# Performance work log

Hardware: AMD Instinct MI355X
Metric: run time of the kernel (lower is better)

Reference implementation:

```python
import jax, jax.numpy as jnp
import numpy as np

KERNEL = 8
STRIDE = 4
HEADS = 8
DIM = 512


def setup_inputs() -> dict:
    key = jax.random.key(0)
    ks = jax.random.split(key, 6)
    B, H, W, C = 8, 64, 64, DIM
    hd = C // HEADS
    return {
        "x": jax.random.normal(ks[0], (B, H, W, C), jnp.float32),
        "w_qkv": jax.random.normal(ks[1], (3 * C, C), jnp.float32) * (C ** -0.5),
        "w_out": jax.random.normal(ks[2], (C, C), jnp.float32) * (C ** -0.5),
        "b_out": jax.random.normal(ks[3], (C,), jnp.float32) * 0.01,
        "rel_h": jax.random.normal(ks[4], (KERNEL, hd), jnp.float32),
        "rel_w": jax.random.normal(ks[5], (KERNEL, hd), jnp.float32),
    }


def reference(x, w_qkv, w_out, b_out, rel_h, rel_w):
    B, H, W, C = x.shape
    k, s, heads = KERNEL, STRIDE, HEADS
    hd = C // heads
    scale = hd ** -0.5
    nH = (H - k) // s + 1
    nW = (W - k) // s + 1
    L = k * k

    # window gather indices
    ii = (jnp.arange(nH) * s)[:, None] + jnp.arange(k)  # [nH, k]
    jj = (jnp.arange(nW) * s)[:, None] + jnp.arange(k)  # [nW, k]
    Ai = ii[:, None, :, None]  # [nH,1,k,1]
    Aj = jj[None, :, None, :]  # [1,nW,1,k]

    win = x[:, Ai, Aj, :]  # [B, nH, nW, k, k, C]
    # faithful to source: permute(0,3,1,2).reshape(B,-1,C) scrambles C into tokens
    xv = jnp.moveaxis(win, -1, 3).reshape(B, nH, nW, L, C)  # [B,nH,nW,L,C]

    qkv = jnp.einsum('bnwlc,oc->bnwlo', xv, w_qkv)  # [B,nH,nW,L,3C]
    q, kk, v = jnp.split(qkv, 3, axis=-1)
    def heads_split(t):
        return t.reshape(B, nH, nW, L, heads, hd)
    q, kk, v = heads_split(q), heads_split(kk), heads_split(v)

    dots = jnp.einsum('bnwlhd,bnwmhd->bnwhlm', q, kk) * scale  # [B,nH,nW,h,L,L]
    # relative bias: (q @ rel^T).sum over kernel axis, broadcast over key dim
    bias_h = jnp.einsum('bnwlhd,kd->bnwhlk', q, rel_h).sum(-1)  # [B,nH,nW,h,L]
    bias_w = jnp.einsum('bnwlhd,kd->bnwhlk', q, rel_w).sum(-1)
    dots = dots + (bias_h + bias_w)[..., None]

    attn = jax.nn.softmax(dots, axis=-1)
    out = jnp.einsum('bnwhlm,bnwmhd->bnwlhd', attn, v).reshape(B, nH, nW, L, C)
    out = jnp.einsum('bnwlc,oc->bnwlo', out, w_out) + b_out  # to_out

    # faithful undo of buggy layout: reshape(B,C,k,k).permute(0,2,3,1)
    out = jnp.moveaxis(out.reshape(B, nH, nW, C, k, k), 3, -1)  # [B,nH,nW,k,k,C]

    res = jnp.zeros_like(x).at[:, Ai, Aj, :].add(out)  # overlapping += accumulation
    return res
```

## Files before the change

kernel.cpp:

```cpp
#include <hip/hip_runtime.h>

#define NHW 15

typedef __bf16 bf16x8 __attribute__((ext_vector_type(8)));
typedef float f32x4 __attribute__((ext_vector_type(4)));
typedef unsigned short u16x8 __attribute__((ext_vector_type(8)));

__device__ __forceinline__ unsigned short f2bf(float f) {
  unsigned x = __float_as_uint(f);
  unsigned r = ((x >> 16) & 1u) + 0x7fffu;
  x += r;
  return (unsigned short)(x >> 16);
}

__device__ __forceinline__ unsigned cvtpk(float lo, float hi) {
  unsigned r;
  asm("v_cvt_pk_bf16_f32 %0, %1, %2" : "=v"(r) : "v"(lo), "v"(hi));
  return r;
}

__global__ void convert_weights(const float* __restrict__ wq,
                                const float* __restrict__ wo,
                                unsigned short* __restrict__ dst) {
  int t = blockIdx.x * 256 + threadIdx.x;
  if (t < 98304) {
    int lane = t & 63, nt = (t >> 6) & 3, ks = (t >> 8) & 15, g = t >> 12;
    int o = g * 64 + nt * 16 + (lane & 15);
    int a = ks * 4 + (lane >> 4);
    const float* src = wq + (size_t)o * 512 + a;
    u16x8 v;
    #pragma unroll
    for (int e = 0; e < 8; ++e) v[e] = f2bf(src[e * 64]);
    *(u16x8*)(dst + (size_t)t * 8) = v;
  } else {
    int u = t - 98304;
    int lane = u & 63, nt = (u >> 6) & 3, ks = (u >> 8) & 15, g = u >> 12;
    int o = g * 64 + nt * 16 + (lane & 15);
    int c0 = ks * 32 + (lane >> 4) * 8;
    const float* src = wo + (size_t)o * 512 + c0;
    float4 v0 = *(const float4*)(src);
    float4 v1 = *(const float4*)(src + 4);
    u16x8 pk;
    pk[0] = f2bf(v0.x); pk[1] = f2bf(v0.y); pk[2] = f2bf(v0.z); pk[3] = f2bf(v0.w);
    pk[4] = f2bf(v1.x); pk[5] = f2bf(v1.y); pk[6] = f2bf(v1.z); pk[7] = f2bf(v1.w);
    *(u16x8*)(dst + 786432 + (size_t)u * 8) = pk;
  }
}

__launch_bounds__(512)
__global__ void swin_kernel(const float* __restrict__ x,
                            const float* __restrict__ b_out,
                            const unsigned short* __restrict__ wq_all,
                            const unsigned short* __restrict__ wo,
                            float* __restrict__ res,
                            int n0, int w0, int nN, int nW, int do_add) {
  __shared__ __align__(16) unsigned short lds0[40960];

  const int tid  = threadIdx.x;
  const int wave = tid >> 6;
  const int ln   = tid & 63;
  const int rowa = ln & 15;
  const int kgrp = ln >> 4;
  const int rbase = kgrp * 4;

  const int bid = blockIdx.x;
  const int b  = bid / (nN * nW);
  const int rm = bid % (nN * nW);
  const int n  = n0 + 2 * (rm / nW);
  const int w  = w0 + 2 * (rm % nW);
  const int i0 = n * 4, j0 = w * 4;

  {
    const float* src = x + (((size_t)(b * 64 + i0)) * 64 + j0 + wave) * 512 + 8 * ln;
    float4 v0[8], v1[8];
    #pragma unroll
    for (int r = 0; r < 8; ++r) {
      v0[r] = *(const float4*)(src + (size_t)r * 32768);
      v1[r] = *(const float4*)(src + (size_t)r * 32768 + 4);
    }
    #pragma unroll
    for (int r = 0; r < 8; ++r) {
      uint4 pk;
      pk.x = cvtpk(v0[r].x, v0[r].y);
      pk.y = cvtpk(v0[r].z, v0[r].w);
      pk.z = cvtpk(v1[r].x, v1[r].y);
      pk.w = cvtpk(v1[r].z, v1[r].w);
      *(uint4*)(lds0 + ln * 520 + (r * 8 + wave) * 8) = pk;
    }
  }
  __syncthreads();

  unsigned qp[4][4][2], kp[4][4][2], vp[4][4][2];
  {
    auto step = [&](int g, unsigned (&dst)[4][4][2]) {
      f32x4 acc[4][4];
      #pragma unroll
      for (int i = 0; i < 4; ++i)
        #pragma unroll
        for (int j = 0; j < 4; ++j) acc[i][j] = (f32x4){0.f, 0.f, 0.f, 0.f};
      const unsigned short* wb = wq_all + (size_t)g * 32768 + ln * 8;
      bf16x8 b0[4], b1[4];
      #pragma unroll
      for (int nt = 0; nt < 4; ++nt) b0[nt] = *(const bf16x8*)(wb + (0 * 4 + nt) * 512);
      #pragma unroll
      for (int nt = 0; nt < 4; ++nt) b1[nt] = *(const bf16x8*)(wb + (1 * 4 + nt) * 512);
      #pragma unroll 1
      for (int ks2 = 0; ks2 < 8; ++ks2) {
        bf16x8 bn0[4], bn1[4];
        if (ks2 < 7) {
          #pragma unroll
          for (int nt = 0; nt < 4; ++nt)
            bn0[nt] = *(const bf16x8*)(wb + ((2 * ks2 + 2) * 4 + nt) * 512);
          #pragma unroll
          for (int nt = 0; nt < 4; ++nt)
            bn1[nt] = *(const bf16x8*)(wb + ((2 * ks2 + 3) * 4 + nt) * 512);
        }
        bf16x8 a[4];
        #pragma unroll
        for (int mt = 0; mt < 4; ++mt)
          a[mt] = *(const bf16x8*)(lds0 + (mt * 16 + rowa) * 520 + (2 * ks2) * 32 + kgrp * 8);
        __builtin_amdgcn_s_setprio(1);
        #pragma unroll
        for (int nt = 0; nt < 4; ++nt)
          #pragma unroll
          for (int mt = 0; mt < 4; ++mt)
            acc[mt][nt] = __builtin_amdgcn_mfma_f32_16x16x32_bf16(a[mt], b0[nt], acc[mt][nt], 0, 0, 0);
        __builtin_amdgcn_s_setprio(0);
        #pragma unroll
        for (int mt = 0; mt < 4; ++mt)
          a[mt] = *(const bf16x8*)(lds0 + (mt * 16 + rowa) * 520 + (2 * ks2 + 1) * 32 + kgrp * 8);
        __builtin_amdgcn_s_setprio(1);
        #pragma unroll
        for (int nt = 0; nt < 4; ++nt)
          #pragma unroll
          for (int mt = 0; mt < 4; ++mt)
            acc[mt][nt] = __builtin_amdgcn_mfma_f32_16x16x32_bf16(a[mt], b1[nt], acc[mt][nt], 0, 0, 0);
        __builtin_amdgcn_s_setprio(0);
        if (ks2 < 7) {
          #pragma unroll
          for (int nt = 0; nt < 4; ++nt) { b0[nt] = bn0[nt]; b1[nt] = bn1[nt]; }
        }
      }
      #pragma unroll
      for (int mt = 0; mt < 4; ++mt)
        #pragma unroll
        for (int nt = 0; nt < 4; ++nt)
          #pragma unroll
          for (int p = 0; p < 2; ++p)
            dst[mt][nt][p] = cvtpk(acc[mt][nt][2 * p], acc[mt][nt][2 * p + 1]);
    };
    step(wave,      qp);
    step(8 + wave,  kp);
    step(16 + wave, vp);
  }
  __syncthreads();

  unsigned short* qsc = lds0 + wave * 5120;
  unsigned short* ksc = qsc + 2560;

  f32x4 dt_[4][4];
  #pragma unroll
  for (int i = 0; i < 4; ++i)
    #pragma unroll
    for (int j = 0; j < 4; ++j) dt_[i][j] = (f32x4){0.f, 0.f, 0.f, 0.f};

  #pragma unroll
  for (int h2 = 0; h2 < 2; ++h2) {
    #pragma unroll
    for (int mt = 0; mt < 4; ++mt)
      #pragma unroll
      for (int cc = 0; cc < 2; ++cc) {
        int ct = 2 * h2 + cc;
        #pragma unroll
        for (int p = 0; p < 2; ++p) {
          unsigned uq = qp[mt][ct][p];
          unsigned uk = kp[mt][ct][p];
          int rr = mt * 16 + rbase + 2 * p;
          int dd = cc * 16 + rowa;
          qsc[rr * 40 + dd]       = (unsigned short)uq;
          qsc[(rr + 1) * 40 + dd] = (unsigned short)(uq >> 16);
          ksc[rr * 40 + dd]       = (unsigned short)uk;
          ksc[(rr + 1) * 40 + dd] = (unsigned short)(uk >> 16);
        }
      }
    bf16x8 aq[4];
    #pragma unroll
    for (int mt = 0; mt < 4; ++mt)
      aq[mt] = *(const bf16x8*)(qsc + (mt * 16 + rowa) * 40 + kgrp * 8);
    __builtin_amdgcn_s_setprio(1);
    #pragma unroll
    for (int nt = 0; nt < 4; ++nt) {
      bf16x8 bk = *(const bf16x8*)(ksc + (nt * 16 + rowa) * 40 + kgrp * 8);
      #pragma unroll
      for (int mt = 0; mt < 4; ++mt)
        dt_[mt][nt] = __builtin_amdgcn_mfma_f32_16x16x32_bf16(aq[mt], bk, dt_[mt][nt], 0, 0, 0);
    }
    __builtin_amdgcn_s_setprio(0);
  }

  const float SC = 0.125f * 1.44269504088896f;
  float rsum[4][4];
  #pragma unroll
  for (int mt = 0; mt < 4; ++mt)
    #pragma unroll
    for (int j = 0; j < 4; ++j) {
      float m = dt_[mt][0][j];
      #pragma unroll
      for (int nt = 1; nt < 4; ++nt) m = fmaxf(m, dt_[mt][nt][j]);
      #pragma unroll
      for (int s = 1; s < 16; s <<= 1) m = fmaxf(m, __shfl_xor(m, s, 64));
      float sum = 0.f;
      #pragma unroll
      for (int nt = 0; nt < 4; ++nt) {
        float p = exp2f((dt_[mt][nt][j] - m) * SC);
        dt_[mt][nt][j] = p;
        sum += p;
      }
      #pragma unroll
      for (int s = 1; s < 16; s <<= 1) sum += __shfl_xor(sum, s, 64);
      rsum[mt][j] = sum;
    }

  unsigned short* Psc  = qsc;
  unsigned short* vTsc = ksc;
  f32x4 oat[4][4];
  #pragma unroll
  for (int i = 0; i < 4; ++i)
    #pragma unroll
    for (int j = 0; j < 4; ++j) oat[i][j] = (f32x4){0.f, 0.f, 0.f, 0.f};

  #pragma unroll
  for (int mh = 0; mh < 2; ++mh) {
    #pragma unroll
    for (int mt = 0; mt < 4; ++mt)
      #pragma unroll
      for (int cc = 0; cc < 2; ++cc) {
        int ct = 2 * mh + cc;
        #pragma unroll
        for (int j = 0; j < 4; ++j)
          Psc[(mt * 16 + rbase + j) * 40 + cc * 16 + rowa] = f2bf(dt_[mt][ct][j]);
      }
    #pragma unroll
    for (int mm = 0; mm < 2; ++mm) {
      int mtm = 2 * mh + mm;
      #pragma unroll
      for (int ct = 0; ct < 4; ++ct)
        #pragma unroll
        for (int p = 0; p < 2; ++p) {
          unsigned u = vp[mtm][ct][p];
          int m_ = mm * 16 + rbase + 2 * p;
          int d  = ct * 16 + rowa;
          *(unsigned*)(vTsc + d * 40 + m_) = u;
        }
    }
    bf16x8 ap[4];
    #pragma unroll
    for (int mt = 0; mt < 4; ++mt)
      ap[mt] = *(const bf16x8*)(Psc + (mt * 16 + rowa) * 40 + kgrp * 8);
    __builtin_amdgcn_s_setprio(1);
    #pragma unroll
    for (int dtt = 0; dtt < 4; ++dtt) {
      bf16x8 bv = *(const bf16x8*)(vTsc + (dtt * 16 + rowa) * 40 + kgrp * 8);
      #pragma unroll
      for (int mt = 0; mt < 4; ++mt)
        oat[mt][dtt] = __builtin_amdgcn_mfma_f32_16x16x32_bf16(ap[mt], bv, oat[mt][dtt], 0, 0, 0);
    }
    __builtin_amdgcn_s_setprio(0);
  }

  #pragma unroll
  for (int mt = 0; mt < 4; ++mt)
    #pragma unroll
    for (int j = 0; j < 4; ++j) {
      float inv = 1.f / rsum[mt][j];
      int l = mt * 16 + rbase + j;
      #pragma unroll
      for (int dtt = 0; dtt < 4; ++dtt)
        qsc[l * 72 + dtt * 16 + rowa] = f2bf(oat[mt][dtt][j] * inv);
    }
  __syncthreads();

  f32x4 a2[4][4];
  #pragma unroll
  for (int i = 0; i < 4; ++i)
    #pragma unroll
    for (int j = 0; j < 4; ++j) a2[i][j] = (f32x4){0.f, 0.f, 0.f, 0.f};
  {
    const unsigned short* wb = wo + (size_t)wave * 32768 + ln * 8;
    bf16x8 b0[4], b1[4];
    #pragma unroll
    for (int nt = 0; nt < 4; ++nt) b0[nt] = *(const bf16x8*)(wb + (0 * 4 + nt) * 512);
    #pragma unroll
    for (int nt = 0; nt < 4; ++nt) b1[nt] = *(const bf16x8*)(wb + (1 * 4 + nt) * 512);
    #pragma unroll 1
    for (int ks2 = 0; ks2 < 8; ++ks2) {
      bf16x8 bn0[4], bn1[4];
      if (ks2 < 7) {
        #pragma unroll
        for (int nt = 0; nt < 4; ++nt)
          bn0[nt] = *(const bf16x8*)(wb + ((2 * ks2 + 2) * 4 + nt) * 512);
        #pragma unroll
        for (int nt = 0; nt < 4; ++nt)
          bn1[nt] = *(const bf16x8*)(wb + ((2 * ks2 + 3) * 4 + nt) * 512);
      }
      bf16x8 a[4];
      #pragma unroll
      for (int mt = 0; mt < 4; ++mt)
        a[mt] = *(const bf16x8*)(lds0 + ks2 * 5120 + (mt * 16 + rowa) * 72 + kgrp * 8);
      __builtin_amdgcn_s_setprio(1);
      #pragma unroll
      for (int nt = 0; nt < 4; ++nt)
        #pragma unroll
        for (int mt = 0; mt < 4; ++mt)
          a2[mt][nt] = __builtin_amdgcn_mfma_f32_16x16x32_bf16(a[mt], b0[nt], a2[mt][nt], 0, 0, 0);
      __builtin_amdgcn_s_setprio(0);
      #pragma unroll
      for (int mt = 0; mt < 4; ++mt)
        a[mt] = *(const bf16x8*)(lds0 + ks2 * 5120 + (mt * 16 + rowa) * 72 + 32 + kgrp * 8);
      __builtin_amdgcn_s_setprio(1);
      #pragma unroll
      for (int nt = 0; nt < 4; ++nt)
        #pragma unroll
        for (int mt = 0; mt < 4; ++mt)
          a2[mt][nt] = __builtin_amdgcn_mfma_f32_16x16x32_bf16(a[mt], b1[nt], a2[mt][nt], 0, 0, 0);
      __builtin_amdgcn_s_setprio(0);
      if (ks2 < 7) {
        #pragma unroll
        for (int nt = 0; nt < 4; ++nt) { b0[nt] = bn0[nt]; b1[nt] = bn1[nt]; }
      }
    }
  }

  float bias[4];
  #pragma unroll
  for (int nt = 0; nt < 4; ++nt) bias[nt] = b_out[wave * 64 + nt * 16 + rowa];

  __syncthreads();

  float* fl = (float*)lds0;
  #pragma unroll
  for (int ph = 0; ph < 2; ++ph) {
    float4 vold[8];
    if (do_add) {
      #pragma unroll
      for (int it = 0; it < 8; ++it) {
        int idx = it * 512 + tid;
        int pp  = idx >> 7;
        int c4  = (idx & 127) << 2;
        int p   = ph * 32 + pp;
        int gh = i0 + (p >> 3), gw = j0 + (p & 7);
        vold[it] = *(const float4*)(res + (((size_t)(b * 64 + gh)) * 64 + gw) * 512 + c4);
      }
    }
    if (ph) __syncthreads();
    #pragma unroll
    for (int nt2 = 0; nt2 < 2; ++nt2) {
      int nt = 2 * ph + nt2;
      int prow = nt2 * 16 + rowa;
      #pragma unroll
      for (int mt = 0; mt < 4; ++mt)
        #pragma unroll
        for (int j = 0; j < 4; ++j) {
          int ch = (mt * 16 + rbase + j) * 8 + wave;
          fl[prow * 517 + ch] = a2[mt][nt][j] + bias[nt];
        }
    }
    __syncthreads();
    #pragma unroll
    for (int it = 0; it < 8; ++it) {
      int idx = it * 512 + tid;
      int pp  = idx >> 7;
      int c4  = (idx & 127) << 2;
      float4 v = *(const float4*)(fl + pp * 517 + c4);
      int p  = ph * 32 + pp;
      int gh = i0 + (p >> 3), gw = j0 + (p & 7);
      float* dst = res + (((size_t)(b * 64 + gh)) * 64 + gw) * 512 + c4;
      if (do_add) {
        v.x += vold[it].x; v.y += vold[it].y; v.z += vold[it].z; v.w += vold[it].w;
      }
      *(float4*)dst = v;
    }
  }
}

extern "C" void kernel_launch(void* const* d_in, const int* in_sizes, int n_in,
                              void* d_out, int out_size, void* d_ws, size_t ws_size,
                              hipStream_t stream) {
  const float* x      = (const float*)d_in[0];
  const float* w_qkv  = (const float*)d_in[1];
  const float* w_out  = (const float*)d_in[2];
  const float* b_out  = (const float*)d_in[3];
  float* res = (float*)d_out;
  unsigned short* wbf = (unsigned short*)d_ws;

  convert_weights<<<512, 256, 0, stream>>>(w_qkv, w_out, wbf);

  const int cls[4][5] = {
      {0, 0, 8, 8, 0},
      {0, 1, 8, 7, 1},
      {1, 0, 7, 8, 1},
      {1, 1, 7, 7, 1},
  };
  for (int c = 0; c < 4; ++c) {
    int nblk = 8 * cls[c][2] * cls[c][3];
    swin_kernel<<<nblk, 512, 0, stream>>>(x, b_out, wbf, wbf + 786432, res,
                                          cls[c][0], cls[c][1], cls[c][2],
                                          cls[c][3], cls[c][4]);
  }
}
```

Before: 380.9 us.

## Split fused window kernel into separate QKV GEMM and attention kernels

Replaces the single fused per-window kernel with two kernels. The first is a QKV projection GEMM that tiles four windows per block across twelve N-blocks and writes bf16 QKV fragments to a workspace buffer. The second is an attention-plus-output-projection kernel that reads those fragments back. The aim is better parallelism and weight reuse in the projection, which dominates the work, at the cost of extra global traffic for the intermediate and more launches. It falls back to the old fused kernel when the workspace is too small.

```diff
diff --git a/kernel.cpp b/kernel.cpp
--- a/kernel.cpp
+++ b/kernel.cpp
@@ -47,6 +47,367 @@
   }
 }
 
+__launch_bounds__(512, 4)
+__global__ void gemm_qkv(const float* __restrict__ x,
+                         const unsigned short* __restrict__ wq_all,
+                         unsigned* __restrict__ qkv,
+                         int n0, int w0, int nN, int nW, int off) {
+  __shared__ __align__(16) unsigned short xs[256 * 72];
+
+  const int tid  = threadIdx.x;
+  const int wave = tid >> 6;
+  const int ln   = tid & 63;
+  const int rowa = ln & 15;
+  const int kgrp = ln >> 4;
+  const int mg = blockIdx.x / 12;
+  const int nb = blockIdx.x % 12;
+  const int awin = wave >> 1;
+  const int wn   = wave & 1;
+  const int g    = nb * 2 + wn;
+
+  int bb[4], i0a[4], j0a[4];
+  {
+    const int nNW = nN * nW;
+    #pragma unroll
+    for (int q = 0; q < 4; ++q) {
+      int rm = off + mg * 4 + q;
+      int b  = rm / nNW;
+      int r1 = rm % nNW;
+      bb[q]  = b;
+      i0a[q] = (n0 + 2 * (r1 / nW)) * 4;
+      j0a[q] = (w0 + 2 * (r1 % nW)) * 4;
+    }
+  }
+
+  f32x4 acc[4][4];
+  #pragma unroll
+  for (int i = 0; i < 4; ++i)
+    #pragma unroll
+    for (int j = 0; j < 4; ++j) acc[i][j] = (f32x4){0.f, 0.f, 0.f, 0.f};
+
+  const unsigned short* wb = wq_all + (size_t)g * 32768 + ln * 8;
+
+  for (int r = 0; r < 8; ++r) {
+    __syncthreads();
+    #pragma unroll
+    for (int q = 0; q < 4; ++q) {
+      const float* src =
+          x + (((size_t)(bb[q] * 64 + i0a[q] + r)) * 64 + j0a[q] + wave) * 512 + 8 * ln;
+      float4 v0 = *(const float4*)(src);
+      float4 v1 = *(const float4*)(src + 4);
+      uint4 pk;
+      pk.x = cvtpk(v0.x, v0.y);
+      pk.y = cvtpk(v0.z, v0.w);
+      pk.z = cvtpk(v1.x, v1.y);
+      pk.w = cvtpk(v1.z, v1.w);
+      *(uint4*)(xs + (q * 64 + ln) * 72 + wave * 8) = pk;
+    }
+    __syncthreads();
+    #pragma unroll
+    for (int kk = 0; kk < 2; ++kk) {
+      const int ks = 2 * r + kk;
+      bf16x8 bfr[4];
+      #pragma unroll
+      for (int nt = 0; nt < 4; ++nt)
+        bfr[nt] = *(const bf16x8*)(wb + (size_t)(ks * 4 + nt) * 512);
+      bf16x8 a[4];
+      #pragma unroll
+      for (int mt = 0; mt < 4; ++mt)
+        a[mt] = *(const bf16x8*)(xs + (awin * 64 + mt * 16 + rowa) * 72 + kk * 32 + kgrp * 8);
+      __builtin_amdgcn_s_setprio(1);
+      #pragma unroll
+      for (int nt = 0; nt < 4; ++nt)
+        #pragma unroll
+        for (int mt = 0; mt < 4; ++mt)
+          acc[mt][nt] = __builtin_amdgcn_mfma_f32_16x16x32_bf16(a[mt], bfr[nt], acc[mt][nt], 0, 0, 0);
+      __builtin_amdgcn_s_setprio(0);
+    }
+  }
+
+  unsigned img[32];
+  #pragma unroll
+  for (int mt = 0; mt < 4; ++mt)
+    #pragma unroll
+    for (int nt = 0; nt < 4; ++nt)
+      #pragma unroll
+      for (int p = 0; p < 2; ++p)
+        img[(mt * 4 + nt) * 2 + p] = cvtpk(acc[mt][nt][2 * p], acc[mt][nt][2 * p + 1]);
+  unsigned* dst = qkv + (((size_t)(mg * 4 + awin) * 24 + g) * 64 + ln) * 32;
+  #pragma unroll
+  for (int k = 0; k < 8; ++k) {
+    uint4 v;
+    v.x = img[4 * k]; v.y = img[4 * k + 1]; v.z = img[4 * k + 2]; v.w = img[4 * k + 3];
+    *(uint4*)(dst + 4 * k) = v;
+  }
+}
+
+__launch_bounds__(512)
+__global__ void attn_kernel(const float* __restrict__ b_out,
+                            const unsigned short* __restrict__ wo,
+                            const unsigned* __restrict__ qkv,
+                            float* __restrict__ res,
+                            int n0, int w0, int nN, int nW, int off, int do_add) {
+  __shared__ __align__(16) unsigned short lds0[40960];
+
+  const int tid  = threadIdx.x;
+  const int wave = tid >> 6;
+  const int ln   = tid & 63;
+  const int rowa = ln & 15;
+  const int kgrp = ln >> 4;
+  const int rbase = kgrp * 4;
+
+  const int rml = blockIdx.x;
+  const int rmg = off + rml;
+  const int b  = rmg / (nN * nW);
+  const int r1 = rmg % (nN * nW);
+  const int n  = n0 + 2 * (r1 / nW);
+  const int w  = w0 + 2 * (r1 % nW);
+  const int i0 = n * 4, j0 = w * 4;
+
+  unsigned qp[4][4][2], kp[4][4][2], vp[4][4][2];
+  {
+    const unsigned* base = qkv + ((size_t)rml * 24 * 64 + ln) * 32;
+    #pragma unroll
+    for (int mt = 0; mt < 4; ++mt)
+      #pragma unroll
+      for (int nt = 0; nt < 4; ++nt)
+        #pragma unroll
+        for (int p = 0; p < 2; ++p) {
+          int idx = (mt * 4 + nt) * 2 + p;
+          qp[mt][nt][p] = base[((size_t)(wave)      * 64) * 32 + idx];
+          kp[mt][nt][p] = base[((size_t)(8 + wave)  * 64) * 32 + idx];
+          vp[mt][nt][p] = base[((size_t)(16 + wave) * 64) * 32 + idx];
+        }
+  }
+
+  unsigned short* qsc = lds0 + wave * 5120;
+  unsigned short* ksc = qsc + 2560;
+
+  f32x4 dt_[4][4];
+  #pragma unroll
+  for (int i = 0; i < 4; ++i)
+    #pragma unroll
+    for (int j = 0; j < 4; ++j) dt_[i][j] = (f32x4){0.f, 0.f, 0.f, 0.f};
+
+  #pragma unroll
+  for (int h2 = 0; h2 < 2; ++h2) {
+    #pragma unroll
+    for (int mt = 0; mt < 4; ++mt)
+      #pragma unroll
+      for (int cc = 0; cc < 2; ++cc) {
+        int ct = 2 * h2 + cc;
+        #pragma unroll
+        for (int p = 0; p < 2; ++p) {
+          unsigned uq = qp[mt][ct][p];
+          unsigned uk = kp[mt][ct][p];
+          int rr = mt * 16 + rbase + 2 * p;
+          int dd = cc * 16 + rowa;
+          qsc[rr * 40 + dd]       = (unsigned short)uq;
+          qsc[(rr + 1) * 40 + dd] = (unsigned short)(uq >> 16);
+          ksc[rr * 40 + dd]       = (unsigned short)uk;
+          ksc[(rr + 1) * 40 + dd] = (unsigned short)(uk >> 16);
+        }
+      }
+    bf16x8 aq[4];
+    #pragma unroll
+    for (int mt = 0; mt < 4; ++mt)
+      aq[mt] = *(const bf16x8*)(qsc + (mt * 16 + rowa) * 40 + kgrp * 8);
+    __builtin_amdgcn_s_setprio(1);
+    #pragma unroll
+    for (int nt = 0; nt < 4; ++nt) {
+      bf16x8 bk = *(const bf16x8*)(ksc + (nt * 16 + rowa) * 40 + kgrp * 8);
+      #pragma unroll
+      for (int mt = 0; mt < 4; ++mt)
+        dt_[mt][nt] = __builtin_amdgcn_mfma_f32_16x16x32_bf16(aq[mt], bk, dt_[mt][nt], 0, 0, 0);
+    }
+    __builtin_amdgcn_s_setprio(0);
+  }
+
+  const float SC = 0.125f * 1.44269504088896f;
+  float rsum[4][4];
+  #pragma unroll
+  for (int mt = 0; mt < 4; ++mt)
+    #pragma unroll
+    for (int j = 0; j < 4; ++j) {
+      float m = dt_[mt][0][j];
+      #pragma unroll
+      for (int nt = 1; nt < 4; ++nt) m = fmaxf(m, dt_[mt][nt][j]);
+      #pragma unroll
+      for (int s = 1; s < 16; s <<= 1) m = fmaxf(m, __shfl_xor(m, s, 64));
+      float sum = 0.f;
+      #pragma unroll
+      for (int nt = 0; nt < 4; ++nt) {
+        float p = exp2f((dt_[mt][nt][j] - m) * SC);
+        dt_[mt][nt][j] = p;
+        sum += p;
+      }
+      #pragma unroll
+      for (int s = 1; s < 16; s <<= 1) sum += __shfl_xor(sum, s, 64);
+      rsum[mt][j] = sum;
+    }
+
+  unsigned short* Psc  = qsc;
+  unsigned short* vTsc = ksc;
+  f32x4 oat[4][4];
+  #pragma unroll
+  for (int i = 0; i < 4; ++i)
+    #pragma unroll
+    for (int j = 0; j < 4; ++j) oat[i][j] = (f32x4){0.f, 0.f, 0.f, 0.f};
+
+  #pragma unroll
+  for (int mh = 0; mh < 2; ++mh) {
+    #pragma unroll
+    for (int mt = 0; mt < 4; ++mt)
+      #pragma unroll
+      for (int cc = 0; cc < 2; ++cc) {
+        int ct = 2 * mh + cc;
+        #pragma unroll
+        for (int j = 0; j < 4; ++j)
+          Psc[(mt * 16 + rbase + j) * 40 + cc * 16 + rowa] = f2bf(dt_[mt][ct][j]);
+      }
+    #pragma unroll
+    for (int mm = 0; mm < 2; ++mm) {
+      int mtm = 2 * mh + mm;
+      #pragma unroll
+      for (int ct = 0; ct < 4; ++ct)
+        #pragma unroll
+        for (int p = 0; p < 2; ++p) {
+          unsigned u = vp[mtm][ct][p];
+          int m_ = mm * 16 + rbase + 2 * p;
+          int d  = ct * 16 + rowa;
+          *(unsigned*)(vTsc + d * 40 + m_) = u;
+        }
+    }
+    bf16x8 ap[4];
+    #pragma unroll
+    for (int mt = 0; mt < 4; ++mt)
+      ap[mt] = *(const bf16x8*)(Psc + (mt * 16 + rowa) * 40 + kgrp * 8);
+    __builtin_amdgcn_s_setprio(1);
+    #pragma unroll
+    for (int dtt = 0; dtt < 4; ++dtt) {
+      bf16x8 bv = *(const bf16x8*)(vTsc + (dtt * 16 + rowa) * 40 + kgrp * 8);
+      #pragma unroll
+      for (int mt = 0; mt < 4; ++mt)
+        oat[mt][dtt] = __builtin_amdgcn_mfma_f32_16x16x32_bf16(ap[mt], bv, oat[mt][dtt], 0, 0, 0);
+    }
+    __builtin_amdgcn_s_setprio(0);
+  }
+
+  #pragma unroll
+  for (int mt = 0; mt < 4; ++mt)
+    #pragma unroll
+    for (int j = 0; j < 4; ++j) {
+      float inv = 1.f / rsum[mt][j];
+      int l = mt * 16 + rbase + j;
+      #pragma unroll
+      for (int dtt = 0; dtt < 4; ++dtt)
+        qsc[l * 72 + dtt * 16 + rowa] = f2bf(oat[mt][dtt][j] * inv);
+    }
+  __syncthreads();
+
+  f32x4 a2[4][4];
+  #pragma unroll
+  for (int i = 0; i < 4; ++i)
+    #pragma unroll
+    for (int j = 0; j < 4; ++j) a2[i][j] = (f32x4){0.f, 0.f, 0.f, 0.f};
+  {
+    const unsigned short* wb = wo + (size_t)wave * 32768 + ln * 8;
+    bf16x8 b0[4], b1[4];
+    #pragma unroll
+    for (int nt = 0; nt < 4; ++nt) b0[nt] = *(const bf16x8*)(wb + (0 * 4 + nt) * 512);
+    #pragma unroll
+    for (int nt = 0; nt < 4; ++nt) b1[nt] = *(const bf16x8*)(wb + (1 * 4 + nt) * 512);
+    #pragma unroll 1
+    for (int ks2 = 0; ks2 < 8; ++ks2) {
+      bf16x8 bn0[4], bn1[4];
+      if (ks2 < 7) {
+        #pragma unroll
+        for (int nt = 0; nt < 4; ++nt)
+          bn0[nt] = *(const bf16x8*)(wb + ((2 * ks2 + 2) * 4 + nt) * 512);
+        #pragma unroll
+        for (int nt = 0; nt < 4; ++nt)
+          bn1[nt] = *(const bf16x8*)(wb + ((2 * ks2 + 3) * 4 + nt) * 512);
+      }
+      bf16x8 a[4];
+      #pragma unroll
+      for (int mt = 0; mt < 4; ++mt)
+        a[mt] = *(const bf16x8*)(lds0 + ks2 * 5120 + (mt * 16 + rowa) * 72 + kgrp * 8);
+      __builtin_amdgcn_s_setprio(1);
+      #pragma unroll
+      for (int nt = 0; nt < 4; ++nt)
+        #pragma unroll
+        for (int mt = 0; mt < 4; ++mt)
+          a2[mt][nt] = __builtin_amdgcn_mfma_f32_16x16x32_bf16(a[mt], b0[nt], a2[mt][nt], 0, 0, 0);
+      __builtin_amdgcn_s_setprio(0);
+      #pragma unroll
+      for (int mt = 0; mt < 4; ++mt)
+        a[mt] = *(const bf16x8*)(lds0 + ks2 * 5120 + (mt * 16 + rowa) * 72 + 32 + kgrp * 8);
+      __builtin_amdgcn_s_setprio(1);
+      #pragma unroll
+      for (int nt = 0; nt < 4; ++nt)
+        #pragma unroll
+        for (int mt = 0; mt < 4; ++mt)
+          a2[mt][nt] = __builtin_amdgcn_mfma_f32_16x16x32_bf16(a[mt], b1[nt], a2[mt][nt], 0, 0, 0);
+      __builtin_amdgcn_s_setprio(0);
+      if (ks2 < 7) {
+        #pragma unroll
+        for (int nt = 0; nt < 4; ++nt) { b0[nt] = bn0[nt]; b1[nt] = bn1[nt]; }
+      }
+    }
+  }
+
+  float bias[4];
+  #pragma unroll
+  for (int nt = 0; nt < 4; ++nt) bias[nt] = b_out[wave * 64 + nt * 16 + rowa];
+
+  __syncthreads();
+
+  float* fl = (float*)lds0;
+  #pragma unroll
+  for (int ph = 0; ph < 2; ++ph) {
+    float4 vold[8];
+    if (do_add) {
+      #pragma unroll
+      for (int it = 0; it < 8; ++it) {
+        int idx = it * 512 + tid;
+        int pp  = idx >> 7;
+        int c4  = (idx & 127) << 2;
+        int p   = ph * 32 + pp;
+        int gh = i0 + (p >> 3), gw = j0 + (p & 7);
+        vold[it] = *(const float4*)(res + (((size_t)(b * 64 + gh)) * 64 + gw) * 512 + c4);
+      }
+    }
+    if (ph) __syncthreads();
+    #pragma unroll
+    for (int nt2 = 0; nt2 < 2; ++nt2) {
+      int nt = 2 * ph + nt2;
+      int prow = nt2 * 16 + rowa;
+      #pragma unroll
+      for (int mt = 0; mt < 4; ++mt)
+        #pragma unroll
+        for (int j = 0; j < 4; ++j) {
+          int ch = (mt * 16 + rbase + j) * 8 + wave;
+          fl[prow * 517 + ch] = a2[mt][nt][j] + bias[nt];
+        }
+    }
+    __syncthreads();
+    #pragma unroll
+    for (int it = 0; it < 8; ++it) {
+      int idx = it * 512 + tid;
+      int pp  = idx >> 7;
+      int c4  = (idx & 127) << 2;
+      float4 v = *(const float4*)(fl + pp * 517 + c4);
+      int p  = ph * 32 + pp;
+      int gh = i0 + (p >> 3), gw = j0 + (p & 7);
+      float* dst = res + (((size_t)(b * 64 + gh)) * 64 + gw) * 512 + c4;
+      if (do_add) {
+        v.x += vold[it].x; v.y += vold[it].y; v.z += vold[it].z; v.w += vold[it].w;
+      }
+      *(float4*)dst = v;
+    }
+  }
+}
+
 __launch_bounds__(512)
 __global__ void swin_kernel(const float* __restrict__ x,
                             const float* __restrict__ b_out,
@@ -392,6 +753,7 @@
   const float* b_out  = (const float*)d_in[3];
   float* res = (float*)d_out;
   unsigned short* wbf = (unsigned short*)d_ws;
+  unsigned* qkvbuf = (unsigned*)((char*)d_ws + (2u << 20));
 
   convert_weights<<<512, 256, 0, stream>>>(w_qkv, w_out, wbf);
 
@@ -401,10 +763,33 @@
       {1, 0, 7, 8, 1},
       {1, 1, 7, 7, 1},
   };
-  for (int c = 0; c < 4; ++c) {
-    int nblk = 8 * cls[c][2] * cls[c][3];
-    swin_kernel<<<nblk, 512, 0, stream>>>(x, b_out, wbf, wbf + 786432, res,
-                                          cls[c][0], cls[c][1], cls[c][2],
-                                          cls[c][3], cls[c][4]);
+
+  const size_t base = (size_t)2 << 20;
+  const size_t per_win = (size_t)24 * 64 * 32 * 4;
+  int chunks;
+  if (ws_size >= base + 512 * per_win)      chunks = 1;
+  else if (ws_size >= base + 256 * per_win) chunks = 2;
+  else                                      chunks = 0;
+
+  if (chunks > 0) {
+    for (int c = 0; c < 4; ++c) {
+      int nwin = 8 * cls[c][2] * cls[c][3];
+      int per = nwin / chunks;
+      for (int h = 0; h < chunks; ++h) {
+        int off = h * per;
+        gemm_qkv<<<(per / 4) * 12, 512, 0, stream>>>(
+            x, wbf, qkvbuf, cls[c][0], cls[c][1], cls[c][2], cls[c][3], off);
+        attn_kernel<<<per, 512, 0, stream>>>(
+            b_out, wbf + 786432, qkvbuf, res,
+            cls[c][0], cls[c][1], cls[c][2], cls[c][3], off, cls[c][4]);
+      }
+    }
+  } else {
+    for (int c = 0; c < 4; ++c) {
+      int nblk = 8 * cls[c][2] * cls[c][3];
+      swin_kernel<<<nblk, 512, 0, stream>>>(x, b_out, wbf, wbf + 786432, res,
+                                            cls[c][0], cls[c][1], cls[c][2],
+                                            cls[c][3], cls[c][4]);
+    }
   }
 }
```

Result: slower. 690.2 us (+81.2%).
